# Performance work log

Hardware: AMD Instinct MI355X
Metric: run time of the kernel (lower is better)

## Reference

```python
import jax, jax.numpy as jnp
import numpy as np

N_NODES = 100000
N_EDGES = 1600000
D_IN = 128
D_OUT = 128


def setup_inputs() -> dict:
    key = jax.random.key(0)
    k1, k2, k3, k4, k5 = jax.random.split(key, 5)
    feat = jax.random.normal(k1, (N_NODES, D_IN), dtype=jnp.float32)
    src = jax.random.randint(k2, (N_EDGES,), 0, N_NODES, dtype=jnp.int32)
    dst = jax.random.randint(k3, (N_EDGES,), 0, N_NODES, dtype=jnp.int32)
    # xavier-ish init for bias-free Linear weights, stored [out, in] like nn.Linear
    scale = float(np.sqrt(2.0 / (D_IN + D_OUT)))
    W_self = jax.random.normal(k4, (D_OUT, D_IN), dtype=jnp.float32) * scale
    W_neigh = jax.random.normal(k5, (D_OUT, D_IN), dtype=jnp.float32) * scale
    return {"feat": feat, "src": src, "dst": dst, "W_self": W_self, "W_neigh": W_neigh}


def reference(feat, src, dst, W_self, W_neigh):
    # SAGEConv, aggregator_type='mean':
    #   h_neigh = mean_{(u->v) in E} feat[u]   (per dst node v)
    #   out = feat @ W_self^T + h_neigh @ W_neigh^T
    n = feat.shape[0]
    msgs = feat[src]  # [E, D_in] gather (dominant memory traffic)
    summed = jax.ops.segment_sum(msgs, dst, num_segments=n)  # [N, D_in]
    deg = jax.ops.segment_sum(jnp.ones((src.shape[0],), feat.dtype), dst, num_segments=n)
    h_neigh = summed / jnp.maximum(deg, 1.0)[:, None]  # zero-degree -> 0 (DGL mean)
    return feat @ W_self.T + h_neigh @ W_neigh.T
```

## Files before the change

kernel.cpp:

```cpp
#include <hip/hip_runtime.h>
#include <hip/hip_bf16.h>

#define D 128
#define KDIM 256
#define BSHIFT 5
#define CPAD 16
#define MAX_BE 768

typedef __attribute__((ext_vector_type(8))) short short8;
typedef __attribute__((ext_vector_type(4))) float floatx4;

static __device__ __forceinline__ ushort f2bf(float x) {
    __hip_bfloat16 h = __float2bfloat16(x);
    return __builtin_bit_cast(ushort, h);
}

__global__ void sage_prep(const float* __restrict__ feat,
                          const float* __restrict__ Wself,
                          const float* __restrict__ Wneigh,
                          ushort* __restrict__ feat_b,
                          ushort* __restrict__ Wc,
                          int nbF, int nFeat8) {
    int b = blockIdx.x;
    if (b < nbF) {
        int i = b * 256 + threadIdx.x;
        if (i < nFeat8) {
            const float4* f4 = (const float4*)feat;
            float4 f0 = f4[(size_t)i * 2];
            float4 f1 = f4[(size_t)i * 2 + 1];
            ushort o[8];
            o[0] = f2bf(f0.x); o[1] = f2bf(f0.y);
            o[2] = f2bf(f0.z); o[3] = f2bf(f0.w);
            o[4] = f2bf(f1.x); o[5] = f2bf(f1.y);
            o[6] = f2bf(f1.z); o[7] = f2bf(f1.w);
            *(short8*)(feat_b + (size_t)i * 8) = *(short8*)o;
        }
    } else {
        int idx = (b - nbF) * 256 + threadIdx.x;
        int j = idx >> 8;
        int k = idx & 255;
        float v = (k < D) ? Wself[j * D + k] : Wneigh[j * D + (k - D)];
        Wc[idx] = f2bf(v);
    }
}

__global__ void bucket_hist(const int* __restrict__ dst,
                            int* __restrict__ bcount,
                            int* __restrict__ rank, int nEdges4) {
    int i = blockIdx.x * blockDim.x + threadIdx.x;
    if (i < nEdges4) {
        int4 d = ((const int4*)dst)[i];
        int4 r;
        r.x = atomicAdd(&bcount[(d.x >> BSHIFT) * CPAD], 1);
        r.y = atomicAdd(&bcount[(d.y >> BSHIFT) * CPAD], 1);
        r.z = atomicAdd(&bcount[(d.z >> BSHIFT) * CPAD], 1);
        r.w = atomicAdd(&bcount[(d.w >> BSHIFT) * CPAD], 1);
        ((int4*)rank)[i] = r;
    }
}

__global__ void bucket_scan(const int* __restrict__ bcount,
                            int* __restrict__ bptr, int nb, int E) {
    __shared__ int s[1024];
    int t = threadIdx.x;
    int base = t * 4;
    int c[4];
#pragma unroll
    for (int j = 0; j < 4; j++)
        c[j] = (base + j < nb) ? bcount[(base + j) * CPAD] : 0;
    int tsum = c[0] + c[1] + c[2] + c[3];
    s[t] = tsum;
    __syncthreads();
#pragma unroll
    for (int off = 1; off < 1024; off <<= 1) {
        int add = (t >= off) ? s[t - off] : 0;
        __syncthreads();
        s[t] += add;
        __syncthreads();
    }
    int run = s[t] - tsum;
#pragma unroll
    for (int j = 0; j < 4; j++) {
        int idx = base + j;
        if (idx < nb) bptr[idx] = run;
        run += c[j];
    }
    if (t == 0) bptr[nb] = E;
}

__global__ void bucket_fill(const int* __restrict__ src, const int* __restrict__ dst,
                            const int* __restrict__ rank,
                            const int* __restrict__ bptr,
                            uint* __restrict__ ep, int nEdges4) {
    int i = blockIdx.x * blockDim.x + threadIdx.x;
    if (i < nEdges4) {
        int4 s = ((const int4*)src)[i];
        int4 d = ((const int4*)dst)[i];
        int4 r = ((const int4*)rank)[i];
        ep[bptr[d.x >> BSHIFT] + r.x] = ((uint)s.x << BSHIFT) | (uint)(d.x & 31);
        ep[bptr[d.y >> BSHIFT] + r.y] = ((uint)s.y << BSHIFT) | (uint)(d.y & 31);
        ep[bptr[d.z >> BSHIFT] + r.z] = ((uint)s.z << BSHIFT) | (uint)(d.z & 31);
        ep[bptr[d.w >> BSHIFT] + r.w] = ((uint)s.w << BSHIFT) | (uint)(d.w & 31);
    }
}

#define ROWS 32
#define LDK 264

__global__ __launch_bounds__(256, 8) void sage_fused(
        const ushort* __restrict__ feat_b,
        const int* __restrict__ bptr,
        const uint* __restrict__ ep,
        const short* __restrict__ Wc,
        float* __restrict__ out,
        int N) {
    __shared__ ushort X[ROWS * LDK];
    __shared__ uint elist[MAX_BE];
    __shared__ int counts[32], offs[32], cur[32];

    const int tid = threadIdx.x;
    const int b = blockIdx.x;
    const int v0 = b * ROWS;

    int e0 = bptr[b];
    int cnt = min(bptr[b + 1] - e0, MAX_BE);

    if (tid < 32) { counts[tid] = 0; cur[tid] = 0; }

#pragma unroll
    for (int i = 0; i < 2; i++) {
        int idx = tid + i * 256;
        int r = idx >> 4;
        int c = idx & 15;
        int v = v0 + r;
        short8 f = {0, 0, 0, 0, 0, 0, 0, 0};
        if (v < N) f = *(const short8*)(feat_b + (size_t)v * D + c * 8);
        *(short8*)&X[r * LDK + c * 8] = f;
    }
    __syncthreads();

    for (int i = tid; i < cnt; i += 256) {
        uint p = ep[e0 + i];
        atomicAdd(&counts[p & 31], 1);
    }
    __syncthreads();
    if (tid == 0) {
        int run = 0;
#pragma unroll
        for (int i = 0; i < 32; i++) { offs[i] = run; run += counts[i]; }
    }
    __syncthreads();
    for (int i = tid; i < cnt; i += 256) {
        uint p = ep[e0 + i];
        int dl = p & 31;
        int slot = offs[dl] + atomicAdd(&cur[dl], 1);
        elist[slot] = p >> BSHIFT;
    }
    __syncthreads();

    {
        const int ln = tid >> 5;
        const int q = tid & 31;
        for (int g = 0; g < 4; g++) {
            int r = g * 8 + ln;
            int v = v0 + r;
            float4 acc = make_float4(0.f, 0.f, 0.f, 0.f);
            float rd = 0.f;
            if (v < N) {
                int dg = counts[r];
                int eb = offs[r];
                rd = (dg > 0) ? 1.0f / (float)dg : 0.f;
                int e = 0;
                for (; e + 7 < dg; e += 8) {
                    uint2 p[8];
#pragma unroll
                    for (int j = 0; j < 8; j++) {
                        uint u = elist[eb + e + j];
                        p[j] = *(const uint2*)(feat_b + (size_t)u * D + q * 4);
                    }
#pragma unroll
                    for (int j = 0; j < 8; j++) {
                        acc.x += __uint_as_float(p[j].x << 16);
                        acc.y += __uint_as_float(p[j].x & 0xffff0000u);
                        acc.z += __uint_as_float(p[j].y << 16);
                        acc.w += __uint_as_float(p[j].y & 0xffff0000u);
                    }
                }
                for (; e + 1 < dg; e += 2) {
                    uint ua = elist[eb + e], ub = elist[eb + e + 1];
                    uint2 pa = *(const uint2*)(feat_b + (size_t)ua * D + q * 4);
                    uint2 pb = *(const uint2*)(feat_b + (size_t)ub * D + q * 4);
                    acc.x += __uint_as_float(pa.x << 16) + __uint_as_float(pb.x << 16);
                    acc.y += __uint_as_float(pa.x & 0xffff0000u) + __uint_as_float(pb.x & 0xffff0000u);
                    acc.z += __uint_as_float(pa.y << 16) + __uint_as_float(pb.y << 16);
                    acc.w += __uint_as_float(pa.y & 0xffff0000u) + __uint_as_float(pb.y & 0xffff0000u);
                }
                if (e < dg) {
                    uint u = elist[eb + e];
                    uint2 pa = *(const uint2*)(feat_b + (size_t)u * D + q * 4);
                    acc.x += __uint_as_float(pa.x << 16);
                    acc.y += __uint_as_float(pa.x & 0xffff0000u);
                    acc.z += __uint_as_float(pa.y << 16);
                    acc.w += __uint_as_float(pa.y & 0xffff0000u);
                }
            }
            ushort o[4];
            o[0] = f2bf(acc.x * rd);
            o[1] = f2bf(acc.y * rd);
            o[2] = f2bf(acc.z * rd);
            o[3] = f2bf(acc.w * rd);
            *(ushort2*)&X[r * LDK + D + q * 4] = *(ushort2*)&o[0];
            *(ushort2*)&X[r * LDK + D + q * 4 + 2] = *(ushort2*)&o[2];
        }
    }
    __syncthreads();

    const int lane = tid & 63;
    const int w = tid >> 6;
    const int col = lane & 15;
    const int quad = lane >> 4;
    const int rowBase = (w & 1) * 16;
    const int ctBase = (w >> 1) * 4;

    floatx4 o[4];
#pragma unroll
    for (int ct = 0; ct < 4; ct++) o[ct] = (floatx4){0.f, 0.f, 0.f, 0.f};

#pragma unroll
    for (int kt = 0; kt < 8; kt++) {
        int k0 = kt * 32;
        short8 a = *(const short8*)&X[(rowBase + col) * LDK + k0 + quad * 8];
#pragma unroll
        for (int ct = 0; ct < 4; ct++) {
            short8 bfr = *(const short8*)(Wc + ((ctBase + ct) * 16 + col) * KDIM + k0 + quad * 8);
            o[ct] = __builtin_amdgcn_mfma_f32_16x16x32_bf16(a, bfr, o[ct], 0, 0, 0);
        }
    }

    int vbase = v0 + rowBase + quad * 4;
#pragma unroll
    for (int ct = 0; ct < 4; ct++) {
#pragma unroll
        for (int r = 0; r < 4; r++) {
            int v = vbase + r;
            if (v < N) out[(size_t)v * D + (ctBase + ct) * 16 + col] = o[ct][r];
        }
    }
}

extern "C" void kernel_launch(void* const* d_in, const int* in_sizes, int n_in,
                              void* d_out, int out_size, void* d_ws, size_t ws_size,
                              hipStream_t stream) {
    const float* feat   = (const float*)d_in[0];
    const int*   src    = (const int*)d_in[1];
    const int*   dst    = (const int*)d_in[2];
    const float* Wself  = (const float*)d_in[3];
    const float* Wneigh = (const float*)d_in[4];
    float* out = (float*)d_out;

    const int N = in_sizes[0] / D;
    const int E = in_sizes[1];
    const int nb = (N + ROWS - 1) / ROWS;

    char* ws = (char*)d_ws;
    size_t off = 0;
    auto carve = [&](size_t bytes) {
        char* p = ws + off;
        off = (off + bytes + 255) & ~(size_t)255;
        return p;
    };
    int*    bcount = (int*)   carve((size_t)nb * CPAD * sizeof(int));
    int*    bptrp  = (int*)   carve((size_t)(nb + 1) * sizeof(int));
    int*    rank   = (int*)   carve((size_t)E * sizeof(int));
    uint*   ep     = (uint*)  carve((size_t)E * sizeof(uint));
    ushort* feat_b = (ushort*)carve((size_t)N * D * sizeof(ushort));
    ushort* Wc     = (ushort*)carve((size_t)D * KDIM * sizeof(ushort));

    const int nFeat8 = N * D / 8;
    const int nbF = (nFeat8 + 255) / 256;

    (void)hipMemsetAsync(bcount, 0, (size_t)nb * CPAD * sizeof(int), stream);

    sage_prep<<<nbF + (D * KDIM) / 256, 256, 0, stream>>>(
        feat, Wself, Wneigh, feat_b, Wc, nbF, nFeat8);

    bucket_hist<<<(E / 4 + 255) / 256, 256, 0, stream>>>(dst, bcount, rank, E / 4);

    bucket_scan<<<1, 1024, 0, stream>>>(bcount, bptrp, nb, E);

    bucket_fill<<<(E / 4 + 255) / 256, 256, 0, stream>>>(src, dst, rank, bptrp,
                                                         ep, E / 4);

    sage_fused<<<nb, 256, 0, stream>>>(feat_b, bptrp, ep, (const short*)Wc, out, N);
}
```

Baseline: 299.6 us.

## Replace global-atomic bucketing with two-pass shared-memory radix partition into CSR

```diff
diff --git a/kernel.cpp b/kernel.cpp
--- a/kernel.cpp
+++ b/kernel.cpp
@@ -3,9 +3,15 @@
 
 #define D 128
 #define KDIM 256
-#define BSHIFT 5
-#define CPAD 16
+#define ROWS 32
+#define LDK 264
 #define MAX_BE 768
+
+#define CSH 9
+#define CWID 512
+#define GFILL 256
+#define FCHUNK 6400
+#define SB_CAP 10240
 
 typedef __attribute__((ext_vector_type(8))) short short8;
 typedef __attribute__((ext_vector_type(4))) float floatx4;
@@ -15,12 +21,15 @@
     return __builtin_bit_cast(ushort, h);
 }
 
-__global__ void sage_prep(const float* __restrict__ feat,
-                          const float* __restrict__ Wself,
-                          const float* __restrict__ Wneigh,
-                          ushort* __restrict__ feat_b,
-                          ushort* __restrict__ Wc,
-                          int nbF, int nFeat8) {
+__global__ void k_prep_hist(const float* __restrict__ feat,
+                            const float* __restrict__ Wself,
+                            const float* __restrict__ Wneigh,
+                            const int* __restrict__ dst,
+                            ushort* __restrict__ feat_b,
+                            ushort* __restrict__ Wc,
+                            int* __restrict__ histA,
+                            int nbF, int nFeat8, int E, int chunk, int nc) {
+    __shared__ int sh[CWID];
     int b = blockIdx.x;
     if (b < nbF) {
         int i = b * 256 + threadIdx.x;
@@ -35,97 +44,180 @@
             o[6] = f2bf(f1.z); o[7] = f2bf(f1.w);
             *(short8*)(feat_b + (size_t)i * 8) = *(short8*)o;
         }
-    } else {
+    } else if (b < nbF + 128) {
         int idx = (b - nbF) * 256 + threadIdx.x;
         int j = idx >> 8;
         int k = idx & 255;
         float v = (k < D) ? Wself[j * D + k] : Wneigh[j * D + (k - D)];
         Wc[idx] = f2bf(v);
-    }
-}
-
-__global__ void bucket_hist(const int* __restrict__ dst,
-                            int* __restrict__ bcount,
-                            int* __restrict__ rank, int nEdges4) {
-    int i = blockIdx.x * blockDim.x + threadIdx.x;
-    if (i < nEdges4) {
-        int4 d = ((const int4*)dst)[i];
-        int4 r;
-        r.x = atomicAdd(&bcount[(d.x >> BSHIFT) * CPAD], 1);
-        r.y = atomicAdd(&bcount[(d.y >> BSHIFT) * CPAD], 1);
-        r.z = atomicAdd(&bcount[(d.z >> BSHIFT) * CPAD], 1);
-        r.w = atomicAdd(&bcount[(d.w >> BSHIFT) * CPAD], 1);
-        ((int4*)rank)[i] = r;
-    }
-}
-
-__global__ void bucket_scan(const int* __restrict__ bcount,
-                            int* __restrict__ bptr, int nb, int E) {
-    __shared__ int s[1024];
+    } else {
+        int b2 = b - nbF - 128;
+        int beg = b2 * chunk;
+        int end = min(E, beg + chunk);
+        for (int i = threadIdx.x; i < nc; i += 256) sh[i] = 0;
+        __syncthreads();
+        for (int i = beg + threadIdx.x; i < end; i += 256)
+            atomicAdd(&sh[((unsigned)dst[i]) >> CSH], 1);
+        __syncthreads();
+        for (int c = threadIdx.x; c < nc; c += 256) histA[c * GFILL + b2] = sh[c];
+    }
+}
+
+__global__ __launch_bounds__(1024) void k_scan(int* __restrict__ histA,
+                                               int* __restrict__ coarsePtr,
+                                               int total, int E) {
+    __shared__ int wsum[16], woff[16];
     int t = threadIdx.x;
-    int base = t * 4;
-    int c[4];
-#pragma unroll
-    for (int j = 0; j < 4; j++)
-        c[j] = (base + j < nb) ? bcount[(base + j) * CPAD] : 0;
-    int tsum = c[0] + c[1] + c[2] + c[3];
-    s[t] = tsum;
-    __syncthreads();
-#pragma unroll
-    for (int off = 1; off < 1024; off <<= 1) {
-        int add = (t >= off) ? s[t - off] : 0;
-        __syncthreads();
-        s[t] += add;
-        __syncthreads();
-    }
-    int run = s[t] - tsum;
-#pragma unroll
-    for (int j = 0; j < 4; j++) {
+    int per = (total + 1023) / 1024;
+    int base = t * per;
+    int tsum = 0;
+    for (int j = 0; j < per; j++) {
         int idx = base + j;
-        if (idx < nb) bptr[idx] = run;
-        run += c[j];
-    }
-    if (t == 0) bptr[nb] = E;
-}
-
-__global__ void bucket_fill(const int* __restrict__ src, const int* __restrict__ dst,
-                            const int* __restrict__ rank,
-                            const int* __restrict__ bptr,
-                            uint* __restrict__ ep, int nEdges4) {
-    int i = blockIdx.x * blockDim.x + threadIdx.x;
-    if (i < nEdges4) {
-        int4 s = ((const int4*)src)[i];
-        int4 d = ((const int4*)dst)[i];
-        int4 r = ((const int4*)rank)[i];
-        ep[bptr[d.x >> BSHIFT] + r.x] = ((uint)s.x << BSHIFT) | (uint)(d.x & 31);
-        ep[bptr[d.y >> BSHIFT] + r.y] = ((uint)s.y << BSHIFT) | (uint)(d.y & 31);
-        ep[bptr[d.z >> BSHIFT] + r.z] = ((uint)s.z << BSHIFT) | (uint)(d.z & 31);
-        ep[bptr[d.w >> BSHIFT] + r.w] = ((uint)s.w << BSHIFT) | (uint)(d.w & 31);
-    }
-}
-
-#define ROWS 32
-#define LDK 264
+        if (idx < total) tsum += histA[idx];
+    }
+    int lane = t & 63, wv = t >> 6;
+    int v = tsum;
+    for (int d = 1; d < 64; d <<= 1) {
+        int o = __shfl_up(v, d, 64);
+        if (lane >= d) v += o;
+    }
+    if (lane == 63) wsum[wv] = v;
+    __syncthreads();
+    if (t == 0) {
+        int run = 0;
+        for (int i = 0; i < 16; i++) { woff[i] = run; run += wsum[i]; }
+    }
+    __syncthreads();
+    int run = (v - tsum) + woff[wv];
+    for (int j = 0; j < per; j++) {
+        int idx = base + j;
+        if (idx < total) {
+            int c = histA[idx];
+            histA[idx] = run;
+            if ((idx & (GFILL - 1)) == 0) coarsePtr[idx / GFILL] = run;
+            run += c;
+        }
+    }
+    if (t == 0) coarsePtr[total / GFILL] = E;
+}
+
+__global__ __launch_bounds__(256) void k_fillA(const int* __restrict__ src,
+                                               const int* __restrict__ dst,
+                                               const int* __restrict__ histA,
+                                               uint* __restrict__ epA,
+                                               int E, int chunk, int nc) {
+    __shared__ int sh[200], soffs[200], scur[200];
+    __shared__ uint sbuf[FCHUNK];
+    int b2 = blockIdx.x;
+    int beg = b2 * chunk;
+    int end = min(E, beg + chunk);
+    int cntB = end - beg;
+    int tid = threadIdx.x;
+    for (int i = tid; i < nc; i += 256) sh[i] = 0;
+    __syncthreads();
+    for (int i = beg + tid; i < end; i += 256)
+        atomicAdd(&sh[((unsigned)dst[i]) >> CSH], 1);
+    __syncthreads();
+    if (tid == 0) {
+        int run = 0;
+        for (int c = 0; c < nc; c++) { soffs[c] = run; run += sh[c]; }
+    }
+    __syncthreads();
+    if (tid < nc) scur[tid] = soffs[tid];
+    __syncthreads();
+    for (int i = beg + tid; i < end; i += 256) {
+        int dv = dst[i];
+        int sv = src[i];
+        int c = ((unsigned)dv) >> CSH;
+        int slot = atomicAdd(&scur[c], 1);
+        sbuf[slot] = ((uint)sv << CSH) | (uint)(dv & (CWID - 1));
+    }
+    __syncthreads();
+    int w = tid >> 6, lane = tid & 63;
+    for (int c = w; c < nc; c += 4) {
+        int s0 = soffs[c];
+        int s1 = (c + 1 < nc) ? soffs[c + 1] : cntB;
+        int gb = histA[c * GFILL + b2];
+        for (int i = s0 + lane; i < s1; i += 64) epA[gb + (i - s0)] = sbuf[i];
+    }
+}
+
+__global__ __launch_bounds__(256) void k_fineB(const uint* __restrict__ epA,
+                                               const int* __restrict__ coarsePtr,
+                                               uint* __restrict__ ep,
+                                               int* __restrict__ nodeptr,
+                                               int nc) {
+    __shared__ uint sbuf[SB_CAP];
+    __shared__ int h[CWID], cur[CWID];
+    __shared__ int wq[4];
+    int c = blockIdx.x;
+    int base = coarsePtr[c];
+    int cnt = min(coarsePtr[c + 1] - base, SB_CAP);
+    int tid = threadIdx.x;
+    int i2 = tid * 2;
+    h[i2] = 0; h[i2 + 1] = 0;
+    __syncthreads();
+    for (int i = tid; i < cnt; i += 256)
+        atomicAdd(&h[epA[base + i] & (CWID - 1)], 1);
+    __syncthreads();
+    int a = h[i2], bb = h[i2 + 1];
+    int pair = a + bb;
+    int lane = tid & 63, wv = tid >> 6;
+    int v = pair;
+    for (int d = 1; d < 64; d <<= 1) {
+        int o = __shfl_up(v, d, 64);
+        if (lane >= d) v += o;
+    }
+    if (lane == 63) wq[wv] = v;
+    __syncthreads();
+    if (tid == 0) {
+        int run = 0;
+        for (int j = 0; j < 4; j++) { int s = wq[j]; wq[j] = run; run += s; }
+    }
+    __syncthreads();
+    int excl = (v - pair) + wq[wv];
+    h[i2] = excl;
+    h[i2 + 1] = excl + a;
+    cur[i2] = excl;
+    cur[i2 + 1] = excl + a;
+    nodeptr[c * CWID + i2] = base + excl;
+    nodeptr[c * CWID + i2 + 1] = base + excl + a;
+    if (tid == 0 && c + 1 == nc) nodeptr[(c + 1) * CWID] = coarsePtr[c + 1];
+    __syncthreads();
+    for (int i = tid; i < cnt; i += 256) {
+        uint p = epA[base + i];
+        int n = p & (CWID - 1);
+        int slot = atomicAdd(&cur[n], 1);
+        sbuf[slot] = p >> CSH;
+    }
+    __syncthreads();
+    for (int i = tid; i < cnt; i += 256) ep[base + i] = sbuf[i];
+}
 
 __global__ __launch_bounds__(256, 8) void sage_fused(
         const ushort* __restrict__ feat_b,
-        const int* __restrict__ bptr,
+        const int* __restrict__ nodeptr,
         const uint* __restrict__ ep,
         const short* __restrict__ Wc,
         float* __restrict__ out,
         int N) {
     __shared__ ushort X[ROWS * LDK];
     __shared__ uint elist[MAX_BE];
-    __shared__ int counts[32], offs[32], cur[32];
+    __shared__ int counts[32], offs[32];
 
     const int tid = threadIdx.x;
     const int b = blockIdx.x;
     const int v0 = b * ROWS;
 
-    int e0 = bptr[b];
-    int cnt = min(bptr[b + 1] - e0, MAX_BE);
-
-    if (tid < 32) { counts[tid] = 0; cur[tid] = 0; }
+    int e0 = nodeptr[v0];
+    int cnt = min(nodeptr[v0 + ROWS] - e0, MAX_BE);
+
+    if (tid < 32) {
+        int np0 = nodeptr[v0 + tid];
+        int np1 = nodeptr[v0 + tid + 1];
+        offs[tid] = np0 - e0;
+        counts[tid] = np1 - np0;
+    }
 
 #pragma unroll
     for (int i = 0; i < 2; i++) {
@@ -137,25 +229,7 @@
         if (v < N) f = *(const short8*)(feat_b + (size_t)v * D + c * 8);
         *(short8*)&X[r * LDK + c * 8] = f;
     }
-    __syncthreads();
-
-    for (int i = tid; i < cnt; i += 256) {
-        uint p = ep[e0 + i];
-        atomicAdd(&counts[p & 31], 1);
-    }
-    __syncthreads();
-    if (tid == 0) {
-        int run = 0;
-#pragma unroll
-        for (int i = 0; i < 32; i++) { offs[i] = run; run += counts[i]; }
-    }
-    __syncthreads();
-    for (int i = tid; i < cnt; i += 256) {
-        uint p = ep[e0 + i];
-        int dl = p & 31;
-        int slot = offs[dl] + atomicAdd(&cur[dl], 1);
-        elist[slot] = p >> BSHIFT;
-    }
+    for (int i = tid; i < cnt; i += 256) elist[i] = ep[e0 + i];
     __syncthreads();
 
     {
@@ -167,24 +241,53 @@
             float4 acc = make_float4(0.f, 0.f, 0.f, 0.f);
             float rd = 0.f;
             if (v < N) {
+                int eb = offs[r];
                 int dg = counts[r];
-                int eb = offs[r];
+                dg = min(dg, max(cnt - eb, 0));
                 rd = (dg > 0) ? 1.0f / (float)dg : 0.f;
                 int e = 0;
-                for (; e + 7 < dg; e += 8) {
-                    uint2 p[8];
+                for (; e + 15 < dg; e += 16) {
+                    uint2 pa[8], pb[8];
 #pragma unroll
                     for (int j = 0; j < 8; j++) {
                         uint u = elist[eb + e + j];
-                        p[j] = *(const uint2*)(feat_b + (size_t)u * D + q * 4);
-                    }
-#pragma unroll
-                    for (int j = 0; j < 8; j++) {
-                        acc.x += __uint_as_float(p[j].x << 16);
-                        acc.y += __uint_as_float(p[j].x & 0xffff0000u);
-                        acc.z += __uint_as_float(p[j].y << 16);
-                        acc.w += __uint_as_float(p[j].y & 0xffff0000u);
-                    }
+                        pa[j] = *(const uint2*)(feat_b + (size_t)u * D + q * 4);
+                    }
+#pragma unroll
+                    for (int j = 0; j < 8; j++) {
+                        uint u = elist[eb + e + 8 + j];
+                        pb[j] = *(const uint2*)(feat_b + (size_t)u * D + q * 4);
+                    }
+#pragma unroll
+                    for (int j = 0; j < 8; j++) {
+                        acc.x += __uint_as_float(pa[j].x << 16);
+                        acc.y += __uint_as_float(pa[j].x & 0xffff0000u);
+                        acc.z += __uint_as_float(pa[j].y << 16);
+                        acc.w += __uint_as_float(pa[j].y & 0xffff0000u);
+                    }
+#pragma unroll
+                    for (int j = 0; j < 8; j++) {
+                        acc.x += __uint_as_float(pb[j].x << 16);
+                        acc.y += __uint_as_float(pb[j].x & 0xffff0000u);
+                        acc.z += __uint_as_float(pb[j].y << 16);
+                        acc.w += __uint_as_float(pb[j].y & 0xffff0000u);
+                    }
+                }
+                if (e + 7 < dg) {
+                    uint2 pa[8];
+#pragma unroll
+                    for (int j = 0; j < 8; j++) {
+                        uint u = elist[eb + e + j];
+                        pa[j] = *(const uint2*)(feat_b + (size_t)u * D + q * 4);
+                    }
+#pragma unroll
+                    for (int j = 0; j < 8; j++) {
+                        acc.x += __uint_as_float(pa[j].x << 16);
+                        acc.y += __uint_as_float(pa[j].x & 0xffff0000u);
+                        acc.z += __uint_as_float(pa[j].y << 16);
+                        acc.w += __uint_as_float(pa[j].y & 0xffff0000u);
+                    }
+                    e += 8;
                 }
                 for (; e + 1 < dg; e += 2) {
                     uint ua = elist[eb + e], ub = elist[eb + e + 1];
@@ -261,6 +364,9 @@
     const int N = in_sizes[0] / D;
     const int E = in_sizes[1];
     const int nb = (N + ROWS - 1) / ROWS;
+    const int nc = (N + CWID - 1) / CWID;
+    const int chunk = (E + GFILL - 1) / GFILL;
+    const int total = nc * GFILL;
 
     char* ws = (char*)d_ws;
     size_t off = 0;
@@ -269,27 +375,25 @@
         off = (off + bytes + 255) & ~(size_t)255;
         return p;
     };
-    int*    bcount = (int*)   carve((size_t)nb * CPAD * sizeof(int));
-    int*    bptrp  = (int*)   carve((size_t)(nb + 1) * sizeof(int));
-    int*    rank   = (int*)   carve((size_t)E * sizeof(int));
-    uint*   ep     = (uint*)  carve((size_t)E * sizeof(uint));
-    ushort* feat_b = (ushort*)carve((size_t)N * D * sizeof(ushort));
-    ushort* Wc     = (ushort*)carve((size_t)D * KDIM * sizeof(ushort));
+    int*    histA    = (int*)   carve((size_t)total * sizeof(int));
+    int*    coarsePtr= (int*)   carve((size_t)(nc + 1) * sizeof(int));
+    uint*   epA      = (uint*)  carve((size_t)E * sizeof(uint));
+    uint*   ep       = (uint*)  carve((size_t)E * sizeof(uint));
+    int*    nodeptr  = (int*)   carve((size_t)(nc * CWID + 1) * sizeof(int));
+    ushort* feat_b   = (ushort*)carve((size_t)N * D * sizeof(ushort));
+    ushort* Wc       = (ushort*)carve((size_t)D * KDIM * sizeof(ushort));
 
     const int nFeat8 = N * D / 8;
     const int nbF = (nFeat8 + 255) / 256;
 
-    (void)hipMemsetAsync(bcount, 0, (size_t)nb * CPAD * sizeof(int), stream);
-
-    sage_prep<<<nbF + (D * KDIM) / 256, 256, 0, stream>>>(
-        feat, Wself, Wneigh, feat_b, Wc, nbF, nFeat8);
-
-    bucket_hist<<<(E / 4 + 255) / 256, 256, 0, stream>>>(dst, bcount, rank, E / 4);
-
-    bucket_scan<<<1, 1024, 0, stream>>>(bcount, bptrp, nb, E);
-
-    bucket_fill<<<(E / 4 + 255) / 256, 256, 0, stream>>>(src, dst, rank, bptrp,
-                                                         ep, E / 4);
-
-    sage_fused<<<nb, 256, 0, stream>>>(feat_b, bptrp, ep, (const short*)Wc, out, N);
-}
+    k_prep_hist<<<nbF + 128 + GFILL, 256, 0, stream>>>(
+        feat, Wself, Wneigh, dst, feat_b, Wc, histA, nbF, nFeat8, E, chunk, nc);
+
+    k_scan<<<1, 1024, 0, stream>>>(histA, coarsePtr, total, E);
+
+    k_fillA<<<GFILL, 256, 0, stream>>>(src, dst, histA, epA, E, chunk, nc);
+
+    k_fineB<<<nc, 256, 0, stream>>>(epA, coarsePtr, ep, nodeptr, nc);
+
+    sage_fused<<<nb, 256, 0, stream>>>(feat_b, nodeptr, ep, (const short*)Wc, out, N);
+}
```

Result: slower. 357.8 us (+19.4%).

## Merge preprocessing kernels into one cooperative kernel with grid syncs

Applied to the files above, without the earlier changes.

```diff
diff --git a/kernel.cpp b/kernel.cpp
--- a/kernel.cpp
+++ b/kernel.cpp
@@ -1,11 +1,18 @@
 #include <hip/hip_runtime.h>
 #include <hip/hip_bf16.h>
+#include <hip/hip_cooperative_groups.h>
+
+namespace cg = cooperative_groups;
 
 #define D 128
 #define KDIM 256
 #define BSHIFT 5
 #define CPAD 16
 #define MAX_BE 768
+#define ROWS 32
+#define LDK 264
+#define GRID_COOP 1024
+#define SCAN_PER 13
 
 typedef __attribute__((ext_vector_type(8))) short short8;
 typedef __attribute__((ext_vector_type(4))) float floatx4;
@@ -15,40 +22,47 @@
     return __builtin_bit_cast(ushort, h);
 }
 
-__global__ void sage_prep(const float* __restrict__ feat,
-                          const float* __restrict__ Wself,
-                          const float* __restrict__ Wneigh,
-                          ushort* __restrict__ feat_b,
-                          ushort* __restrict__ Wc,
-                          int nbF, int nFeat8) {
-    int b = blockIdx.x;
-    if (b < nbF) {
-        int i = b * 256 + threadIdx.x;
-        if (i < nFeat8) {
-            const float4* f4 = (const float4*)feat;
-            float4 f0 = f4[(size_t)i * 2];
-            float4 f1 = f4[(size_t)i * 2 + 1];
-            ushort o[8];
-            o[0] = f2bf(f0.x); o[1] = f2bf(f0.y);
-            o[2] = f2bf(f0.z); o[3] = f2bf(f0.w);
-            o[4] = f2bf(f1.x); o[5] = f2bf(f1.y);
-            o[6] = f2bf(f1.z); o[7] = f2bf(f1.w);
-            *(short8*)(feat_b + (size_t)i * 8) = *(short8*)o;
-        }
-    } else {
-        int idx = (b - nbF) * 256 + threadIdx.x;
+__global__ __launch_bounds__(256) void k_pipeline(
+        const float* __restrict__ feat,
+        const float* __restrict__ Wself,
+        const float* __restrict__ Wneigh,
+        const int* __restrict__ src,
+        const int* __restrict__ dst,
+        ushort* __restrict__ feat_b,
+        ushort* __restrict__ Wc,
+        int* __restrict__ bcount,
+        int* __restrict__ bptr,
+        int* __restrict__ rank,
+        uint* __restrict__ ep,
+        int nFeat8, int E, int nb) {
+    cg::grid_group grid = cg::this_grid();
+    __shared__ int wsum[4];
+
+    const int gtid = blockIdx.x * 256 + threadIdx.x;
+    const int nthr = gridDim.x * 256;
+    const int E4 = E >> 2;
+
+    for (int i = gtid; i < nb * CPAD; i += nthr) bcount[i] = 0;
+    grid.sync();
+
+    for (int i = gtid; i < nFeat8; i += nthr) {
+        const float4* f4 = (const float4*)feat;
+        float4 f0 = f4[(size_t)i * 2];
+        float4 f1 = f4[(size_t)i * 2 + 1];
+        ushort o[8];
+        o[0] = f2bf(f0.x); o[1] = f2bf(f0.y);
+        o[2] = f2bf(f0.z); o[3] = f2bf(f0.w);
+        o[4] = f2bf(f1.x); o[5] = f2bf(f1.y);
+        o[6] = f2bf(f1.z); o[7] = f2bf(f1.w);
+        *(short8*)(feat_b + (size_t)i * 8) = *(short8*)o;
+    }
+    for (int idx = gtid; idx < D * KDIM; idx += nthr) {
         int j = idx >> 8;
         int k = idx & 255;
         float v = (k < D) ? Wself[j * D + k] : Wneigh[j * D + (k - D)];
         Wc[idx] = f2bf(v);
     }
-}
-
-__global__ void bucket_hist(const int* __restrict__ dst,
-                            int* __restrict__ bcount,
-                            int* __restrict__ rank, int nEdges4) {
-    int i = blockIdx.x * blockDim.x + threadIdx.x;
-    if (i < nEdges4) {
+    for (int i = gtid; i < E4; i += nthr) {
         int4 d = ((const int4*)dst)[i];
         int4 r;
         r.x = atomicAdd(&bcount[(d.x >> BSHIFT) * CPAD], 1);
@@ -57,43 +71,46 @@
         r.w = atomicAdd(&bcount[(d.w >> BSHIFT) * CPAD], 1);
         ((int4*)rank)[i] = r;
     }
-}
-
-__global__ void bucket_scan(const int* __restrict__ bcount,
-                            int* __restrict__ bptr, int nb, int E) {
-    __shared__ int s[1024];
-    int t = threadIdx.x;
-    int base = t * 4;
-    int c[4];
-#pragma unroll
-    for (int j = 0; j < 4; j++)
-        c[j] = (base + j < nb) ? bcount[(base + j) * CPAD] : 0;
-    int tsum = c[0] + c[1] + c[2] + c[3];
-    s[t] = tsum;
-    __syncthreads();
-#pragma unroll
-    for (int off = 1; off < 1024; off <<= 1) {
-        int add = (t >= off) ? s[t - off] : 0;
+    grid.sync();
+
+    if (blockIdx.x == 0) {
+        int t = threadIdx.x;
+        int base = t * SCAN_PER;
+        int c[SCAN_PER];
+        int tsum = 0;
+#pragma unroll
+        for (int j = 0; j < SCAN_PER; j++) {
+            int idx = base + j;
+            c[j] = (idx < nb) ? bcount[idx * CPAD] : 0;
+            tsum += c[j];
+        }
+        int lane = t & 63, wv = t >> 6;
+        int v = tsum;
+#pragma unroll
+        for (int d2 = 1; d2 < 64; d2 <<= 1) {
+            int o = __shfl_up(v, d2, 64);
+            if (lane >= d2) v += o;
+        }
+        if (lane == 63) wsum[wv] = v;
         __syncthreads();
-        s[t] += add;
+        if (t == 0) {
+            int run = 0;
+#pragma unroll
+            for (int j = 0; j < 4; j++) { int s = wsum[j]; wsum[j] = run; run += s; }
+        }
         __syncthreads();
-    }
-    int run = s[t] - tsum;
-#pragma unroll
-    for (int j = 0; j < 4; j++) {
-        int idx = base + j;
-        if (idx < nb) bptr[idx] = run;
-        run += c[j];
-    }
-    if (t == 0) bptr[nb] = E;
-}
-
-__global__ void bucket_fill(const int* __restrict__ src, const int* __restrict__ dst,
-                            const int* __restrict__ rank,
-                            const int* __restrict__ bptr,
-                            uint* __restrict__ ep, int nEdges4) {
-    int i = blockIdx.x * blockDim.x + threadIdx.x;
-    if (i < nEdges4) {
+        int run = (v - tsum) + wsum[wv];
+#pragma unroll
+        for (int j = 0; j < SCAN_PER; j++) {
+            int idx = base + j;
+            if (idx < nb) bptr[idx] = run;
+            run += c[j];
+        }
+        if (t == 0) bptr[nb] = E;
+    }
+    grid.sync();
+
+    for (int i = gtid; i < E4; i += nthr) {
         int4 s = ((const int4*)src)[i];
         int4 d = ((const int4*)dst)[i];
         int4 r = ((const int4*)rank)[i];
@@ -103,9 +120,6 @@
         ep[bptr[d.w >> BSHIFT] + r.w] = ((uint)s.w << BSHIFT) | (uint)(d.w & 31);
     }
 }
-
-#define ROWS 32
-#define LDK 264
 
 __global__ __launch_bounds__(256, 8) void sage_fused(
         const ushort* __restrict__ feat_b,
@@ -258,9 +272,9 @@
     const float* Wneigh = (const float*)d_in[4];
     float* out = (float*)d_out;
 
-    const int N = in_sizes[0] / D;
-    const int E = in_sizes[1];
-    const int nb = (N + ROWS - 1) / ROWS;
+    int N = in_sizes[0] / D;
+    int E = in_sizes[1];
+    int nb = (N + ROWS - 1) / ROWS;
 
     char* ws = (char*)d_ws;
     size_t off = 0;
@@ -276,20 +290,18 @@
     ushort* feat_b = (ushort*)carve((size_t)N * D * sizeof(ushort));
     ushort* Wc     = (ushort*)carve((size_t)D * KDIM * sizeof(ushort));
 
-    const int nFeat8 = N * D / 8;
-    const int nbF = (nFeat8 + 255) / 256;
-
-    (void)hipMemsetAsync(bcount, 0, (size_t)nb * CPAD * sizeof(int), stream);
-
-    sage_prep<<<nbF + (D * KDIM) / 256, 256, 0, stream>>>(
-        feat, Wself, Wneigh, feat_b, Wc, nbF, nFeat8);
-
-    bucket_hist<<<(E / 4 + 255) / 256, 256, 0, stream>>>(dst, bcount, rank, E / 4);
-
-    bucket_scan<<<1, 1024, 0, stream>>>(bcount, bptrp, nb, E);
-
-    bucket_fill<<<(E / 4 + 255) / 256, 256, 0, stream>>>(src, dst, rank, bptrp,
-                                                         ep, E / 4);
+    int nFeat8 = N * D / 8;
+
+    void* args[] = {
+        (void*)&feat, (void*)&Wself, (void*)&Wneigh,
+        (void*)&src, (void*)&dst,
+        (void*)&feat_b, (void*)&Wc,
+        (void*)&bcount, (void*)&bptrp, (void*)&rank, (void*)&ep,
+        (void*)&nFeat8, (void*)&E, (void*)&nb
+    };
+    (void)hipLaunchCooperativeKernel((const void*)k_pipeline,
+                                     dim3(GRID_COOP), dim3(256),
+                                     args, 0, stream);
 
     sage_fused<<<nb, 256, 0, stream>>>(feat_b, bptrp, ep, (const short*)Wc, out, N);
 }
```

Result: slower. 573.6 us (+91.5%).

## Replace histogram-scan-fill bucketing with fixed-capacity bucket scatter fused into prep

Applied to the files above, without the earlier changes.

```diff
diff --git a/kernel.cpp b/kernel.cpp
--- a/kernel.cpp
+++ b/kernel.cpp
@@ -6,6 +6,8 @@
 #define BSHIFT 5
 #define CPAD 16
 #define MAX_BE 768
+#define ROWS 32
+#define LDK 264
 
 typedef __attribute__((ext_vector_type(8))) short short8;
 typedef __attribute__((ext_vector_type(4))) float floatx4;
@@ -15,12 +17,17 @@
     return __builtin_bit_cast(ushort, h);
 }
 
-__global__ void sage_prep(const float* __restrict__ feat,
-                          const float* __restrict__ Wself,
-                          const float* __restrict__ Wneigh,
-                          ushort* __restrict__ feat_b,
-                          ushort* __restrict__ Wc,
-                          int nbF, int nFeat8) {
+__global__ __launch_bounds__(256) void k_prep_scatter(
+        const float* __restrict__ feat,
+        const float* __restrict__ Wself,
+        const float* __restrict__ Wneigh,
+        const int* __restrict__ src,
+        const int* __restrict__ dst,
+        ushort* __restrict__ feat_b,
+        ushort* __restrict__ Wc,
+        int* __restrict__ bcount,
+        uint* __restrict__ ep,
+        int nbF, int nFeat8, int E4) {
     int b = blockIdx.x;
     if (b < nbF) {
         int i = b * 256 + threadIdx.x;
@@ -35,81 +42,41 @@
             o[6] = f2bf(f1.z); o[7] = f2bf(f1.w);
             *(short8*)(feat_b + (size_t)i * 8) = *(short8*)o;
         }
-    } else {
+    } else if (b < nbF + 128) {
         int idx = (b - nbF) * 256 + threadIdx.x;
         int j = idx >> 8;
         int k = idx & 255;
         float v = (k < D) ? Wself[j * D + k] : Wneigh[j * D + (k - D)];
         Wc[idx] = f2bf(v);
-    }
-}
-
-__global__ void bucket_hist(const int* __restrict__ dst,
-                            int* __restrict__ bcount,
-                            int* __restrict__ rank, int nEdges4) {
-    int i = blockIdx.x * blockDim.x + threadIdx.x;
-    if (i < nEdges4) {
-        int4 d = ((const int4*)dst)[i];
-        int4 r;
-        r.x = atomicAdd(&bcount[(d.x >> BSHIFT) * CPAD], 1);
-        r.y = atomicAdd(&bcount[(d.y >> BSHIFT) * CPAD], 1);
-        r.z = atomicAdd(&bcount[(d.z >> BSHIFT) * CPAD], 1);
-        r.w = atomicAdd(&bcount[(d.w >> BSHIFT) * CPAD], 1);
-        ((int4*)rank)[i] = r;
-    }
-}
-
-__global__ void bucket_scan(const int* __restrict__ bcount,
-                            int* __restrict__ bptr, int nb, int E) {
-    __shared__ int s[1024];
-    int t = threadIdx.x;
-    int base = t * 4;
-    int c[4];
-#pragma unroll
-    for (int j = 0; j < 4; j++)
-        c[j] = (base + j < nb) ? bcount[(base + j) * CPAD] : 0;
-    int tsum = c[0] + c[1] + c[2] + c[3];
-    s[t] = tsum;
-    __syncthreads();
-#pragma unroll
-    for (int off = 1; off < 1024; off <<= 1) {
-        int add = (t >= off) ? s[t - off] : 0;
-        __syncthreads();
-        s[t] += add;
-        __syncthreads();
-    }
-    int run = s[t] - tsum;
-#pragma unroll
-    for (int j = 0; j < 4; j++) {
-        int idx = base + j;
-        if (idx < nb) bptr[idx] = run;
-        run += c[j];
-    }
-    if (t == 0) bptr[nb] = E;
-}
-
-__global__ void bucket_fill(const int* __restrict__ src, const int* __restrict__ dst,
-                            const int* __restrict__ rank,
-                            const int* __restrict__ bptr,
-                            uint* __restrict__ ep, int nEdges4) {
-    int i = blockIdx.x * blockDim.x + threadIdx.x;
-    if (i < nEdges4) {
-        int4 s = ((const int4*)src)[i];
-        int4 d = ((const int4*)dst)[i];
-        int4 r = ((const int4*)rank)[i];
-        ep[bptr[d.x >> BSHIFT] + r.x] = ((uint)s.x << BSHIFT) | (uint)(d.x & 31);
-        ep[bptr[d.y >> BSHIFT] + r.y] = ((uint)s.y << BSHIFT) | (uint)(d.y & 31);
-        ep[bptr[d.z >> BSHIFT] + r.z] = ((uint)s.z << BSHIFT) | (uint)(d.z & 31);
-        ep[bptr[d.w >> BSHIFT] + r.w] = ((uint)s.w << BSHIFT) | (uint)(d.w & 31);
-    }
-}
-
-#define ROWS 32
-#define LDK 264
+    } else {
+        int i = (b - nbF - 128) * 256 + threadIdx.x;
+        if (i < E4) {
+            int4 s = ((const int4*)src)[i];
+            int4 d = ((const int4*)dst)[i];
+            int bx, slot;
+            bx = d.x >> BSHIFT;
+            slot = atomicAdd(&bcount[bx * CPAD], 1);
+            if (slot < MAX_BE)
+                ep[(size_t)bx * MAX_BE + slot] = ((uint)s.x << BSHIFT) | (uint)(d.x & 31);
+            bx = d.y >> BSHIFT;
+            slot = atomicAdd(&bcount[bx * CPAD], 1);
+            if (slot < MAX_BE)
+                ep[(size_t)bx * MAX_BE + slot] = ((uint)s.y << BSHIFT) | (uint)(d.y & 31);
+            bx = d.z >> BSHIFT;
+            slot = atomicAdd(&bcount[bx * CPAD], 1);
+            if (slot < MAX_BE)
+                ep[(size_t)bx * MAX_BE + slot] = ((uint)s.z << BSHIFT) | (uint)(d.z & 31);
+            bx = d.w >> BSHIFT;
+            slot = atomicAdd(&bcount[bx * CPAD], 1);
+            if (slot < MAX_BE)
+                ep[(size_t)bx * MAX_BE + slot] = ((uint)s.w << BSHIFT) | (uint)(d.w & 31);
+        }
+    }
+}
 
 __global__ __launch_bounds__(256, 8) void sage_fused(
         const ushort* __restrict__ feat_b,
-        const int* __restrict__ bptr,
+        const int* __restrict__ bcount,
         const uint* __restrict__ ep,
         const short* __restrict__ Wc,
         float* __restrict__ out,
@@ -122,8 +89,8 @@
     const int b = blockIdx.x;
     const int v0 = b * ROWS;
 
-    int e0 = bptr[b];
-    int cnt = min(bptr[b + 1] - e0, MAX_BE);
+    const int e0 = b * MAX_BE;
+    int cnt = min(bcount[b * CPAD], MAX_BE);
 
     if (tid < 32) { counts[tid] = 0; cur[tid] = 0; }
 
@@ -270,26 +237,20 @@
         return p;
     };
     int*    bcount = (int*)   carve((size_t)nb * CPAD * sizeof(int));
-    int*    bptrp  = (int*)   carve((size_t)(nb + 1) * sizeof(int));
-    int*    rank   = (int*)   carve((size_t)E * sizeof(int));
-    uint*   ep     = (uint*)  carve((size_t)E * sizeof(uint));
+    uint*   ep     = (uint*)  carve((size_t)nb * MAX_BE * sizeof(uint));
     ushort* feat_b = (ushort*)carve((size_t)N * D * sizeof(ushort));
     ushort* Wc     = (ushort*)carve((size_t)D * KDIM * sizeof(ushort));
 
     const int nFeat8 = N * D / 8;
     const int nbF = (nFeat8 + 255) / 256;
+    const int E4 = E / 4;
+    const int nScat = (E4 + 255) / 256;
 
     (void)hipMemsetAsync(bcount, 0, (size_t)nb * CPAD * sizeof(int), stream);
 
-    sage_prep<<<nbF + (D * KDIM) / 256, 256, 0, stream>>>(
-        feat, Wself, Wneigh, feat_b, Wc, nbF, nFeat8);
-
-    bucket_hist<<<(E / 4 + 255) / 256, 256, 0, stream>>>(dst, bcount, rank, E / 4);
-
-    bucket_scan<<<1, 1024, 0, stream>>>(bcount, bptrp, nb, E);
-
-    bucket_fill<<<(E / 4 + 255) / 256, 256, 0, stream>>>(src, dst, rank, bptrp,
-                                                         ep, E / 4);
-
-    sage_fused<<<nb, 256, 0, stream>>>(feat_b, bptrp, ep, (const short*)Wc, out, N);
-}
+    k_prep_scatter<<<nbF + 128 + nScat, 256, 0, stream>>>(
+        feat, Wself, Wneigh, src, dst, feat_b, Wc, bcount, ep,
+        nbF, nFeat8, E4);
+
+    sage_fused<<<nb, 256, 0, stream>>>(feat_b, bcount, ep, (const short*)Wc, out, N);
+}
```

Result: faster. 287.9 us (-3.9%).
